# Optimization experiments

Hardware: AMD Instinct MI355X
Metric: run time of the kernel (lower is better)

The kernel has to match this reference:

```python
import jax, jax.numpy as jnp
import numpy as np
from jax import lax

B, C, H_CH, G = 4, 16, 128, 64
STOCH_RATE = 0.5
TWO_PI = np.float32(2.0 * np.pi)
ALIVE_THRESH = np.float32(0.1)


def _sobel_percep_kernel(c):
    # depthwise perception: [identity, sobel_x, sobel_y, sobel_z] per channel
    s = np.array([1.0, 2.0, 1.0], np.float32)
    d = np.array([-1.0, 0.0, 1.0], np.float32)
    ident = np.zeros((3, 3, 3), np.float32); ident[1, 1, 1] = 1.0
    sx = np.einsum('i,j,k->ijk', s, s, d)
    sy = np.einsum('i,j,k->ijk', s, d, s)
    sz = np.einsum('i,j,k->ijk', d, s, s)
    base = np.stack([ident, sx, sy, sz], 0)          # [4,3,3,3]
    k = np.tile(base, (c, 1, 1, 1))                  # [4C,3,3,3], group-major
    return jnp.asarray(k.reshape(4 * c, 1, 3, 3, 3))


def setup_inputs() -> dict:
    key = jax.random.key(0)
    k1, k2, k3, k4, k5 = jax.random.split(key, 5)
    x = jax.random.normal(k1, (B, C, G, G, G), jnp.float32)
    percep_kernel = _sobel_percep_kernel(C)          # [4C,1,3,3,3] fixed sobel stencils
    W1 = jax.random.normal(k2, (H_CH, 4 * C), jnp.float32) * 0.1
    b1 = jax.random.normal(k3, (H_CH,), jnp.float32) * 0.1
    W2 = jax.random.normal(k4, (C, H_CH), jnp.float32) * 0.1
    stoch_mask = jax.random.uniform(k5, (B, 1, G, G, G), jnp.float32)
    return {"x": x, "percep_kernel": percep_kernel, "W1": W1, "b1": b1,
            "W2": W2, "stoch_mask": stoch_mask}


def reference(x, percep_kernel, W1, b1, W2, stoch_mask):
    # alive mask: max_pool3d(alpha, k=3, s=1, p=1) > 0.1
    alpha = x[:, 3:4]
    pooled = lax.reduce_window(alpha, -jnp.inf, lax.max,
                               (1, 1, 3, 3, 3), (1, 1, 1, 1, 1), 'SAME')
    alive = (pooled > ALIVE_THRESH).astype(x.dtype)  # [B,1,D,H,W]
    # perception: depthwise 3x3x3 conv, 4 filters per channel
    p = lax.conv_general_dilated(x, percep_kernel, (1, 1, 1), 'SAME',
                                 feature_group_count=C,
                                 dimension_numbers=('NCDHW', 'OIDHW', 'NCDHW'))
    # per-voxel MLP: conv1 (1x1x1, bias) -> relu -> conv2 (1x1x1, no bias)
    h = jax.nn.relu(jnp.einsum('oc,bcdhw->bodhw', W1, p)
                    + b1[None, :, None, None, None])
    dx = jnp.einsum('oc,bcdhw->bodhw', W2, h)
    # stochastic residual update
    smask = (stoch_mask <= STOCH_RATE).astype(x.dtype)
    xn = x + dx * smask
    # orientation_channels == 1: mask states, wrap angle channel mod 2*pi
    states = xn[:, :-1] * alive
    angle = jnp.mod(xn[:, -1:], TWO_PI)
    return jnp.concatenate([states, angle], axis=1)
```

## Files before the change

### kernel.cpp

```cpp
#include <hip/hip_runtime.h>
#include <math.h>

#define Bc 4
#define Cc 16
#define Hc 128
#define Gc 64

#define TZ 4
#define TY 4
#define TXX 16
#define HZ (TZ + 2)
#define HY (TY + 2)
#define HXX (TXX + 2)
#define HALO_PER_C (HZ * HY * HXX)
#define CH_PER_PASS 8

__global__ __launch_bounds__(256, 2) void nca_fused(
    const float* __restrict__ x,
    const float* __restrict__ W1,
    const float* __restrict__ b1,
    const float* __restrict__ W2,
    const float* __restrict__ stoch,
    float* __restrict__ out)
{
    __shared__ float w1s[Hc * 64];
    __shared__ float w2ts[Hc * Cc];
    __shared__ float b1s[Hc];
    __shared__ float xs[CH_PER_PASS * HALO_PER_C];

    const int tid = threadIdx.x;

    int bid = blockIdx.x;
    const int xt = bid % (Gc / TXX); bid /= (Gc / TXX);
    const int yt = bid % (Gc / TY); bid /= (Gc / TY);
    const int zt = bid % (Gc / TZ); bid /= (Gc / TZ);
    const int b  = bid;

    const int z0 = zt * TZ, y0 = yt * TY, x0 = xt * TXX;

    {
        const float4* W1v = (const float4*)W1;
        float4* w1sv = (float4*)w1s;
#pragma unroll
        for (int i = 0; i < (Hc * 64 / 4) / 256; ++i)
            w1sv[tid + i * 256] = W1v[tid + i * 256];
        if (tid < Hc) b1s[tid] = b1[tid];
#pragma unroll
        for (int i = 0; i < (Cc * Hc) / 256; ++i) {
            const int idx = tid + i * 256;
            const int k = idx >> 7;
            const int h = idx & (Hc - 1);
            w2ts[h * Cc + k] = W2[idx];
        }
    }

    const int tx = tid % TXX;
    const int ty = (tid / TXX) % TY;
    const int tz = tid / (TXX * TY);

    float p[64];
    float pooled = -1e30f;

#pragma unroll
    for (int pass = 0; pass < 2; ++pass) {
        __syncthreads();
        for (int idx = tid; idx < CH_PER_PASS * HALO_PER_C; idx += 256) {
            int hx = idx % HXX;
            int t  = idx / HXX;
            int hy = t % HY; t /= HY;
            int hz = t % HZ;
            int cc = t / HZ;
            const int c = pass * CH_PER_PASS + cc;
            int gz = z0 + hz - 1, gy = y0 + hy - 1, gx = x0 + hx - 1;
            float v = 0.0f;
            if ((unsigned)gz < (unsigned)Gc && (unsigned)gy < (unsigned)Gc &&
                (unsigned)gx < (unsigned)Gc) {
                v = x[(((b * Cc + c) * Gc + gz) * Gc + gy) * Gc + gx];
            }
            xs[idx] = v;
        }
        __syncthreads();

#pragma unroll
        for (int cc = 0; cc < CH_PER_PASS; ++cc) {
            const int g = pass * CH_PER_PASS + cc;
            const float* xc = &xs[cc * HALO_PER_C];
            float S[3][3], D[3][3];
            float center = 0.0f;
#pragma unroll
            for (int dz = 0; dz < 3; ++dz) {
#pragma unroll
                for (int dy = 0; dy < 3; ++dy) {
                    const int base = (tz + dz) * (HY * HXX) + (ty + dy) * HXX + tx;
                    const float a  = xc[base + 0];
                    const float m  = xc[base + 1];
                    const float c2 = xc[base + 2];
                    S[dz][dy] = a + 2.0f * m + c2;
                    D[dz][dy] = c2 - a;
                    if (dz == 1 && dy == 1) center = m;
                    if (g == 3) pooled = fmaxf(pooled, fmaxf(fmaxf(a, m), c2));
                }
            }
            const float sx = (D[0][0] + 2.0f * D[0][1] + D[0][2])
                     + 2.0f * (D[1][0] + 2.0f * D[1][1] + D[1][2])
                     +        (D[2][0] + 2.0f * D[2][1] + D[2][2]);
            const float sy = (S[0][2] - S[0][0])
                     + 2.0f * (S[1][2] - S[1][0])
                     +        (S[2][2] - S[2][0]);
            const float sz = (S[2][0] + 2.0f * S[2][1] + S[2][2])
                           - (S[0][0] + 2.0f * S[0][1] + S[0][2]);
            p[4 * g + 0] = center;
            p[4 * g + 1] = sx;
            p[4 * g + 2] = sy;
            p[4 * g + 3] = sz;
        }
    }

    const float alive = (pooled > 0.1f) ? 1.0f : 0.0f;

    float dxv[16];
#pragma unroll
    for (int k = 0; k < 16; ++k) dxv[k] = 0.0f;

#pragma unroll 1
    for (int o = 0; o < Hc; o += 8) {
        float acc[8];
#pragma unroll
        for (int i = 0; i < 8; ++i) acc[i] = b1s[o + i];
#pragma unroll
        for (int i = 0; i < 8; ++i) {
            const float4* w4 = (const float4*)&w1s[(o + i) * 64];
#pragma unroll
            for (int c4 = 0; c4 < 16; ++c4) {
                const float4 w = w4[c4];
                acc[i] = fmaf(w.x, p[4 * c4 + 0], acc[i]);
                acc[i] = fmaf(w.y, p[4 * c4 + 1], acc[i]);
                acc[i] = fmaf(w.z, p[4 * c4 + 2], acc[i]);
                acc[i] = fmaf(w.w, p[4 * c4 + 3], acc[i]);
            }
        }
#pragma unroll
        for (int i = 0; i < 8; ++i) {
            const float h = fmaxf(acc[i], 0.0f);
            const float4* w2 = (const float4*)&w2ts[(o + i) * Cc];
#pragma unroll
            for (int k4 = 0; k4 < 4; ++k4) {
                const float4 w = w2[k4];
                dxv[4 * k4 + 0] = fmaf(w.x, h, dxv[4 * k4 + 0]);
                dxv[4 * k4 + 1] = fmaf(w.y, h, dxv[4 * k4 + 1]);
                dxv[4 * k4 + 2] = fmaf(w.z, h, dxv[4 * k4 + 2]);
                dxv[4 * k4 + 3] = fmaf(w.w, h, dxv[4 * k4 + 3]);
            }
        }
    }

    const int gz = z0 + tz, gy = y0 + ty, gx = x0 + tx;
    const int vox = ((b * Gc + gz) * Gc + gy) * Gc + gx;
    const float sm = (stoch[vox] <= 0.5f) ? 1.0f : 0.0f;

    const float TWO_PI_F = 6.2831854820251464844f;

#pragma unroll
    for (int k = 0; k < 16; ++k) {
        const float xn = p[4 * k] + dxv[k] * sm;
        float res;
        if (k < 15) {
            res = xn * alive;
        } else {
            res = fmodf(xn, TWO_PI_F);
            if (res < 0.0f) res += TWO_PI_F;
        }
        out[(((b * Cc + k) * Gc + gz) * Gc + gy) * Gc + gx] = res;
    }
}

extern "C" void kernel_launch(void* const* d_in, const int* in_sizes, int n_in,
                              void* d_out, int out_size, void* d_ws, size_t ws_size,
                              hipStream_t stream) {
    const float* x     = (const float*)d_in[0];
    const float* W1    = (const float*)d_in[2];
    const float* b1    = (const float*)d_in[3];
    const float* W2    = (const float*)d_in[4];
    const float* stoch = (const float*)d_in[5];
    float* out = (float*)d_out;

    const int nblocks = Bc * (Gc / TZ) * (Gc / TY) * (Gc / TXX);
    nca_fused<<<nblocks, 256, 0, stream>>>(x, W1, b1, W2, stoch, out);
}
```

Measured before the change: 602.6 us.

## Compute two voxels per thread to reuse shared-memory weight loads in MLP

New measurement: 996.2 us. +65.3%, slower.

```diff
diff --git a/kernel.cpp b/kernel.cpp
--- a/kernel.cpp
+++ b/kernel.cpp
@@ -8,12 +8,14 @@
 
 #define TZ 4
 #define TY 4
-#define TXX 16
+#define TXH 16
+#define TXX 32
 #define HZ (TZ + 2)
 #define HY (TY + 2)
 #define HXX (TXX + 2)
 #define HALO_PER_C (HZ * HY * HXX)
-#define CH_PER_PASS 8
+#define CH_PER_PASS 4
+#define NPASS (Cc / CH_PER_PASS)
 
 __global__ __launch_bounds__(256, 2) void nca_fused(
     const float* __restrict__ x,
@@ -31,9 +33,9 @@
     const int tid = threadIdx.x;
 
     int bid = blockIdx.x;
-    const int xt = bid % (Gc / TXX); bid /= (Gc / TXX);
-    const int yt = bid % (Gc / TY); bid /= (Gc / TY);
-    const int zt = bid % (Gc / TZ); bid /= (Gc / TZ);
+    const int xt = bid & 1; bid >>= 1;
+    const int yt = bid & 15; bid >>= 4;
+    const int zt = bid & 15; bid >>= 4;
     const int b  = bid;
 
     const int z0 = zt * TZ, y0 = yt * TY, x0 = xt * TXX;
@@ -54,15 +56,15 @@
         }
     }
 
-    const int tx = tid % TXX;
-    const int ty = (tid / TXX) % TY;
-    const int tz = tid / (TXX * TY);
-
-    float p[64];
-    float pooled = -1e30f;
-
-#pragma unroll
-    for (int pass = 0; pass < 2; ++pass) {
+    const int tx = tid & 15;
+    const int ty = (tid >> 4) & 3;
+    const int tz = tid >> 6;
+
+    float p0[64], p1[64];
+    float pool0 = -1e30f, pool1 = -1e30f;
+
+#pragma unroll
+    for (int pass = 0; pass < NPASS; ++pass) {
         __syncthreads();
         for (int idx = tid; idx < CH_PER_PASS * HALO_PER_C; idx += 256) {
             int hx = idx % HXX;
@@ -85,92 +87,135 @@
         for (int cc = 0; cc < CH_PER_PASS; ++cc) {
             const int g = pass * CH_PER_PASS + cc;
             const float* xc = &xs[cc * HALO_PER_C];
-            float S[3][3], D[3][3];
-            float center = 0.0f;
+            float S0[3][3], D0[3][3], S1[3][3], D1[3][3];
+            float c0 = 0.0f, c1 = 0.0f;
 #pragma unroll
             for (int dz = 0; dz < 3; ++dz) {
 #pragma unroll
                 for (int dy = 0; dy < 3; ++dy) {
                     const int base = (tz + dz) * (HY * HXX) + (ty + dy) * HXX + tx;
-                    const float a  = xc[base + 0];
-                    const float m  = xc[base + 1];
-                    const float c2 = xc[base + 2];
-                    S[dz][dy] = a + 2.0f * m + c2;
-                    D[dz][dy] = c2 - a;
-                    if (dz == 1 && dy == 1) center = m;
-                    if (g == 3) pooled = fmaxf(pooled, fmaxf(fmaxf(a, m), c2));
+                    const float a0 = xc[base + 0];
+                    const float m0 = xc[base + 1];
+                    const float q0 = xc[base + 2];
+                    const float a1 = xc[base + 16];
+                    const float m1 = xc[base + 17];
+                    const float q1 = xc[base + 18];
+                    S0[dz][dy] = a0 + 2.0f * m0 + q0;
+                    D0[dz][dy] = q0 - a0;
+                    S1[dz][dy] = a1 + 2.0f * m1 + q1;
+                    D1[dz][dy] = q1 - a1;
+                    if (dz == 1 && dy == 1) { c0 = m0; c1 = m1; }
+                    if (g == 3) {
+                        pool0 = fmaxf(pool0, fmaxf(fmaxf(a0, m0), q0));
+                        pool1 = fmaxf(pool1, fmaxf(fmaxf(a1, m1), q1));
+                    }
                 }
             }
-            const float sx = (D[0][0] + 2.0f * D[0][1] + D[0][2])
-                     + 2.0f * (D[1][0] + 2.0f * D[1][1] + D[1][2])
-                     +        (D[2][0] + 2.0f * D[2][1] + D[2][2]);
-            const float sy = (S[0][2] - S[0][0])
-                     + 2.0f * (S[1][2] - S[1][0])
-                     +        (S[2][2] - S[2][0]);
-            const float sz = (S[2][0] + 2.0f * S[2][1] + S[2][2])
-                           - (S[0][0] + 2.0f * S[0][1] + S[0][2]);
-            p[4 * g + 0] = center;
-            p[4 * g + 1] = sx;
-            p[4 * g + 2] = sy;
-            p[4 * g + 3] = sz;
-        }
-    }
-
-    const float alive = (pooled > 0.1f) ? 1.0f : 0.0f;
-
-    float dxv[16];
-#pragma unroll
-    for (int k = 0; k < 16; ++k) dxv[k] = 0.0f;
+            const float sx0 = (D0[0][0] + 2.0f * D0[0][1] + D0[0][2])
+                      + 2.0f * (D0[1][0] + 2.0f * D0[1][1] + D0[1][2])
+                      +        (D0[2][0] + 2.0f * D0[2][1] + D0[2][2]);
+            const float sy0 = (S0[0][2] - S0[0][0])
+                      + 2.0f * (S0[1][2] - S0[1][0])
+                      +        (S0[2][2] - S0[2][0]);
+            const float sz0 = (S0[2][0] + 2.0f * S0[2][1] + S0[2][2])
+                            - (S0[0][0] + 2.0f * S0[0][1] + S0[0][2]);
+            const float sx1 = (D1[0][0] + 2.0f * D1[0][1] + D1[0][2])
+                      + 2.0f * (D1[1][0] + 2.0f * D1[1][1] + D1[1][2])
+                      +        (D1[2][0] + 2.0f * D1[2][1] + D1[2][2]);
+            const float sy1 = (S1[0][2] - S1[0][0])
+                      + 2.0f * (S1[1][2] - S1[1][0])
+                      +        (S1[2][2] - S1[2][0]);
+            const float sz1 = (S1[2][0] + 2.0f * S1[2][1] + S1[2][2])
+                            - (S1[0][0] + 2.0f * S1[0][1] + S1[0][2]);
+            p0[4 * g + 0] = c0; p0[4 * g + 1] = sx0;
+            p0[4 * g + 2] = sy0; p0[4 * g + 3] = sz0;
+            p1[4 * g + 0] = c1; p1[4 * g + 1] = sx1;
+            p1[4 * g + 2] = sy1; p1[4 * g + 3] = sz1;
+        }
+    }
+
+    const float alive0 = (pool0 > 0.1f) ? 1.0f : 0.0f;
+    const float alive1 = (pool1 > 0.1f) ? 1.0f : 0.0f;
+
+    float dx0[16], dx1[16];
+#pragma unroll
+    for (int k = 0; k < 16; ++k) { dx0[k] = 0.0f; dx1[k] = 0.0f; }
+
+    const float4* w1sv  = (const float4*)w1s;
+    const float4* w2tsv = (const float4*)w2ts;
+    const float4* b1sv  = (const float4*)b1s;
 
 #pragma unroll 1
     for (int o = 0; o < Hc; o += 8) {
-        float acc[8];
-#pragma unroll
-        for (int i = 0; i < 8; ++i) acc[i] = b1s[o + i];
+        float acc0[8], acc1[8];
+        {
+            const float4 ba = b1sv[(o >> 2) + 0];
+            const float4 bb = b1sv[(o >> 2) + 1];
+            acc0[0] = ba.x; acc0[1] = ba.y; acc0[2] = ba.z; acc0[3] = ba.w;
+            acc0[4] = bb.x; acc0[5] = bb.y; acc0[6] = bb.z; acc0[7] = bb.w;
+#pragma unroll
+            for (int i = 0; i < 8; ++i) acc1[i] = acc0[i];
+        }
+        const float4* wb = w1sv + o * 16;
+#pragma unroll
+        for (int c4 = 0; c4 < 16; ++c4) {
+#pragma unroll
+            for (int i = 0; i < 8; ++i) {
+                const float4 w = wb[i * 16 + c4];
+                acc0[i] = fmaf(w.x, p0[4 * c4 + 0], acc0[i]);
+                acc0[i] = fmaf(w.y, p0[4 * c4 + 1], acc0[i]);
+                acc0[i] = fmaf(w.z, p0[4 * c4 + 2], acc0[i]);
+                acc0[i] = fmaf(w.w, p0[4 * c4 + 3], acc0[i]);
+                acc1[i] = fmaf(w.x, p1[4 * c4 + 0], acc1[i]);
+                acc1[i] = fmaf(w.y, p1[4 * c4 + 1], acc1[i]);
+                acc1[i] = fmaf(w.z, p1[4 * c4 + 2], acc1[i]);
+                acc1[i] = fmaf(w.w, p1[4 * c4 + 3], acc1[i]);
+            }
+        }
+        const float4* w2b = w2tsv + o * 4;
 #pragma unroll
         for (int i = 0; i < 8; ++i) {
-            const float4* w4 = (const float4*)&w1s[(o + i) * 64];
-#pragma unroll
-            for (int c4 = 0; c4 < 16; ++c4) {
-                const float4 w = w4[c4];
-                acc[i] = fmaf(w.x, p[4 * c4 + 0], acc[i]);
-                acc[i] = fmaf(w.y, p[4 * c4 + 1], acc[i]);
-                acc[i] = fmaf(w.z, p[4 * c4 + 2], acc[i]);
-                acc[i] = fmaf(w.w, p[4 * c4 + 3], acc[i]);
-            }
-        }
-#pragma unroll
-        for (int i = 0; i < 8; ++i) {
-            const float h = fmaxf(acc[i], 0.0f);
-            const float4* w2 = (const float4*)&w2ts[(o + i) * Cc];
+            const float h0 = fmaxf(acc0[i], 0.0f);
+            const float h1 = fmaxf(acc1[i], 0.0f);
 #pragma unroll
             for (int k4 = 0; k4 < 4; ++k4) {
-                const float4 w = w2[k4];
-                dxv[4 * k4 + 0] = fmaf(w.x, h, dxv[4 * k4 + 0]);
-                dxv[4 * k4 + 1] = fmaf(w.y, h, dxv[4 * k4 + 1]);
-                dxv[4 * k4 + 2] = fmaf(w.z, h, dxv[4 * k4 + 2]);
-                dxv[4 * k4 + 3] = fmaf(w.w, h, dxv[4 * k4 + 3]);
-            }
-        }
-    }
-
-    const int gz = z0 + tz, gy = y0 + ty, gx = x0 + tx;
-    const int vox = ((b * Gc + gz) * Gc + gy) * Gc + gx;
-    const float sm = (stoch[vox] <= 0.5f) ? 1.0f : 0.0f;
+                const float4 w = w2b[i * 4 + k4];
+                dx0[4 * k4 + 0] = fmaf(w.x, h0, dx0[4 * k4 + 0]);
+                dx0[4 * k4 + 1] = fmaf(w.y, h0, dx0[4 * k4 + 1]);
+                dx0[4 * k4 + 2] = fmaf(w.z, h0, dx0[4 * k4 + 2]);
+                dx0[4 * k4 + 3] = fmaf(w.w, h0, dx0[4 * k4 + 3]);
+                dx1[4 * k4 + 0] = fmaf(w.x, h1, dx1[4 * k4 + 0]);
+                dx1[4 * k4 + 1] = fmaf(w.y, h1, dx1[4 * k4 + 1]);
+                dx1[4 * k4 + 2] = fmaf(w.z, h1, dx1[4 * k4 + 2]);
+                dx1[4 * k4 + 3] = fmaf(w.w, h1, dx1[4 * k4 + 3]);
+            }
+        }
+    }
+
+    const int gz = z0 + tz, gy = y0 + ty;
+    const int gx0 = x0 + tx, gx1 = x0 + tx + 16;
+    const int vox0 = ((b * Gc + gz) * Gc + gy) * Gc + gx0;
+    const int vox1 = vox0 + 16;
+    const float sm0 = (stoch[vox0] <= 0.5f) ? 1.0f : 0.0f;
+    const float sm1 = (stoch[vox1] <= 0.5f) ? 1.0f : 0.0f;
 
     const float TWO_PI_F = 6.2831854820251464844f;
 
+    const int obase = (((b * Cc) * Gc + gz) * Gc + gy) * Gc;
 #pragma unroll
     for (int k = 0; k < 16; ++k) {
-        const float xn = p[4 * k] + dxv[k] * sm;
-        float res;
+        const float xn0 = p0[4 * k] + dx0[k] * sm0;
+        const float xn1 = p1[4 * k] + dx1[k] * sm1;
+        float r0, r1;
         if (k < 15) {
-            res = xn * alive;
+            r0 = xn0 * alive0;
+            r1 = xn1 * alive1;
         } else {
-            res = fmodf(xn, TWO_PI_F);
-            if (res < 0.0f) res += TWO_PI_F;
-        }
-        out[(((b * Cc + k) * Gc + gz) * Gc + gy) * Gc + gx] = res;
+            r0 = fmodf(xn0, TWO_PI_F); if (r0 < 0.0f) r0 += TWO_PI_F;
+            r1 = fmodf(xn1, TWO_PI_F); if (r1 < 0.0f) r1 += TWO_PI_F;
+        }
+        out[obase + k * (Gc * Gc * Gc) + gx0] = r0;
+        out[obase + k * (Gc * Gc * Gc) + gx1] = r1;
     }
 }
 
```

## Move per-voxel MLP onto bf16 MFMA with three-way split for fp32 accuracy

Applied to the files above, without the earlier changes.

New measurement: 1.033 ms. +71.5%, slower.

```diff
diff --git a/kernel.cpp b/kernel.cpp
--- a/kernel.cpp
+++ b/kernel.cpp
@@ -7,15 +7,47 @@
 #define Gc 64
 
 #define TZ 4
-#define TY 4
-#define TXX 16
-#define HZ (TZ + 2)
-#define HY (TY + 2)
-#define HXX (TXX + 2)
-#define HALO_PER_C (HZ * HY * HXX)
-#define CH_PER_PASS 8
-
-__global__ __launch_bounds__(256, 2) void nca_fused(
+#define TY 8
+#define TX 8
+#define HALO 600
+
+typedef __attribute__((ext_vector_type(8)))  short        short8;
+typedef __attribute__((ext_vector_type(16))) float        f32x16;
+typedef __attribute__((ext_vector_type(4)))  unsigned int uint4v;
+typedef __attribute__((ext_vector_type(2)))  int          int2v;
+
+union FragU { uint4v u4; short8 s8; unsigned int u[4]; };
+
+static __device__ __forceinline__ unsigned int cvt_pk_bf16(float a, float b) {
+    unsigned int r;
+    asm("v_cvt_pk_bf16_f32 %0, %1, %2" : "=v"(r) : "v"(a), "v"(b));
+    return r;
+}
+static __device__ __forceinline__ void swap32(unsigned int &a, unsigned int &b) {
+    int2v r = __builtin_amdgcn_permlane32_swap((int)a, (int)b, false, false);
+    a = (unsigned int)r.x;
+    b = (unsigned int)r.y;
+}
+static __device__ __forceinline__ float lo_bf(unsigned int w) {
+    union { unsigned int u; float f; } x; x.u = w << 16; return x.f;
+}
+static __device__ __forceinline__ float hi_bf(unsigned int w) {
+    union { unsigned int u; float f; } x; x.u = w & 0xffff0000u; return x.f;
+}
+static __device__ __forceinline__ void split3(float a, float b,
+                                              unsigned int &wh, unsigned int &wm,
+                                              unsigned int &wl) {
+    wh = cvt_pk_bf16(a, b);
+    float r0 = a - lo_bf(wh), r1 = b - hi_bf(wh);
+    wm = cvt_pk_bf16(r0, r1);
+    r0 -= lo_bf(wm); r1 -= hi_bf(wm);
+    wl = cvt_pk_bf16(r0, r1);
+}
+static __device__ __forceinline__ f32x16 MF(const FragU& A, const FragU& B, f32x16 C) {
+    return __builtin_amdgcn_mfma_f32_32x32x16_bf16(A.s8, B.s8, C, 0, 0, 0);
+}
+
+__global__ __launch_bounds__(256, 2) void nca_mfma(
     const float* __restrict__ x,
     const float* __restrict__ W1,
     const float* __restrict__ b1,
@@ -23,154 +55,243 @@
     const float* __restrict__ stoch,
     float* __restrict__ out)
 {
-    __shared__ float w1s[Hc * 64];
-    __shared__ float w2ts[Hc * Cc];
-    __shared__ float b1s[Hc];
-    __shared__ float xs[CH_PER_PASS * HALO_PER_C];
-
-    const int tid = threadIdx.x;
+    __shared__ uint4v w1f[48 * 64];
+    __shared__ uint4v w2f[24 * 32];
+    __shared__ float  b1s[Hc];
+    __shared__ float  xs[HALO];
+
+    const int tid  = threadIdx.x;
+    const int lane = tid & 63;
 
     int bid = blockIdx.x;
-    const int xt = bid % (Gc / TXX); bid /= (Gc / TXX);
-    const int yt = bid % (Gc / TY); bid /= (Gc / TY);
-    const int zt = bid % (Gc / TZ); bid /= (Gc / TZ);
+    const int xt = bid & 7;  bid >>= 3;
+    const int yt = bid & 7;  bid >>= 3;
+    const int zt = bid & 15; bid >>= 4;
     const int b  = bid;
-
-    const int z0 = zt * TZ, y0 = yt * TY, x0 = xt * TXX;
-
-    {
-        const float4* W1v = (const float4*)W1;
-        float4* w1sv = (float4*)w1s;
-#pragma unroll
-        for (int i = 0; i < (Hc * 64 / 4) / 256; ++i)
-            w1sv[tid + i * 256] = W1v[tid + i * 256];
-        if (tid < Hc) b1s[tid] = b1[tid];
-#pragma unroll
-        for (int i = 0; i < (Cc * Hc) / 256; ++i) {
-            const int idx = tid + i * 256;
-            const int k = idx >> 7;
-            const int h = idx & (Hc - 1);
-            w2ts[h * Cc + k] = W2[idx];
-        }
-    }
-
-    const int tx = tid % TXX;
-    const int ty = (tid / TXX) % TY;
-    const int tz = tid / (TXX * TY);
+    const int z0 = zt * TZ, y0 = yt * TY, x0 = xt * TX;
+
+#pragma unroll
+    for (int i = 0; i < 4; ++i) {
+        const int slot = tid + i * 256;
+        const int L  = slot & 63;
+        const int ks = (slot >> 6) & 3;
+        const int t  = slot >> 8;
+        const int row = 32 * t + (L & 31);
+        const int kb  = 16 * ks + 8 * (L >> 5);
+        const float* src = W1 + row * 64 + kb;
+        unsigned int h[4], m[4], l[4];
+#pragma unroll
+        for (int q = 0; q < 4; ++q) split3(src[2*q], src[2*q+1], h[q], m[q], l[q]);
+        w1f[((t*4+ks)*3+0)*64 + L] = (uint4v){h[0],h[1],h[2],h[3]};
+        w1f[((t*4+ks)*3+1)*64 + L] = (uint4v){m[0],m[1],m[2],m[3]};
+        w1f[((t*4+ks)*3+2)*64 + L] = (uint4v){l[0],l[1],l[2],l[3]};
+    }
+#pragma unroll
+    for (int i = 0; i < 3; ++i) {
+        const int e = tid + i * 256;
+        const int sub = e & 31, slot = e >> 5;
+        const int ks = slot / 3, lvl = slot % 3;
+        const int r = sub & 15, hh = sub >> 4;
+        const int kb = 16 * ks + 8 * hh;
+        const float* src = W2 + r * Hc + kb;
+        unsigned int w[4];
+#pragma unroll
+        for (int q = 0; q < 4; ++q) {
+            unsigned int h, m, l;
+            split3(src[2*q], src[2*q+1], h, m, l);
+            w[q] = (lvl == 0) ? h : ((lvl == 1) ? m : l);
+        }
+        w2f[slot*32 + sub] = (uint4v){w[0],w[1],w[2],w[3]};
+    }
+    if (tid < Hc) b1s[tid] = b1[tid];
+
+    const int tx = tid & 7;
+    const int ty = (tid >> 3) & 7;
+    const int tz = tid >> 6;
 
     float p[64];
     float pooled = -1e30f;
 
 #pragma unroll
-    for (int pass = 0; pass < 2; ++pass) {
+    for (int c = 0; c < 16; ++c) {
         __syncthreads();
-        for (int idx = tid; idx < CH_PER_PASS * HALO_PER_C; idx += 256) {
-            int hx = idx % HXX;
-            int t  = idx / HXX;
-            int hy = t % HY; t /= HY;
-            int hz = t % HZ;
-            int cc = t / HZ;
-            const int c = pass * CH_PER_PASS + cc;
-            int gz = z0 + hz - 1, gy = y0 + hy - 1, gx = x0 + hx - 1;
+        for (int idx = tid; idx < HALO; idx += 256) {
+            const int hz = idx / 100;
+            const int r2 = idx - hz * 100;
+            const int hy = r2 / 10;
+            const int hx = r2 - hy * 10;
+            const int gz = z0 + hz - 1, gy = y0 + hy - 1, gx = x0 + hx - 1;
             float v = 0.0f;
             if ((unsigned)gz < (unsigned)Gc && (unsigned)gy < (unsigned)Gc &&
-                (unsigned)gx < (unsigned)Gc) {
-                v = x[(((b * Cc + c) * Gc + gz) * Gc + gy) * Gc + gx];
-            }
+                (unsigned)gx < (unsigned)Gc)
+                v = x[(((b*Cc + c)*Gc + gz)*Gc + gy)*Gc + gx];
             xs[idx] = v;
         }
         __syncthreads();
-
-#pragma unroll
-        for (int cc = 0; cc < CH_PER_PASS; ++cc) {
-            const int g = pass * CH_PER_PASS + cc;
-            const float* xc = &xs[cc * HALO_PER_C];
-            float S[3][3], D[3][3];
-            float center = 0.0f;
-#pragma unroll
-            for (int dz = 0; dz < 3; ++dz) {
-#pragma unroll
-                for (int dy = 0; dy < 3; ++dy) {
-                    const int base = (tz + dz) * (HY * HXX) + (ty + dy) * HXX + tx;
-                    const float a  = xc[base + 0];
-                    const float m  = xc[base + 1];
-                    const float c2 = xc[base + 2];
-                    S[dz][dy] = a + 2.0f * m + c2;
-                    D[dz][dy] = c2 - a;
-                    if (dz == 1 && dy == 1) center = m;
-                    if (g == 3) pooled = fmaxf(pooled, fmaxf(fmaxf(a, m), c2));
-                }
-            }
-            const float sx = (D[0][0] + 2.0f * D[0][1] + D[0][2])
-                     + 2.0f * (D[1][0] + 2.0f * D[1][1] + D[1][2])
-                     +        (D[2][0] + 2.0f * D[2][1] + D[2][2]);
-            const float sy = (S[0][2] - S[0][0])
-                     + 2.0f * (S[1][2] - S[1][0])
-                     +        (S[2][2] - S[2][0]);
-            const float sz = (S[2][0] + 2.0f * S[2][1] + S[2][2])
-                           - (S[0][0] + 2.0f * S[0][1] + S[0][2]);
-            p[4 * g + 0] = center;
-            p[4 * g + 1] = sx;
-            p[4 * g + 2] = sy;
-            p[4 * g + 3] = sz;
-        }
-    }
-
-    const float alive = (pooled > 0.1f) ? 1.0f : 0.0f;
+        float S[3][3], D[3][3], center = 0.f;
+#pragma unroll
+        for (int dz = 0; dz < 3; ++dz)
+#pragma unroll
+            for (int dy = 0; dy < 3; ++dy) {
+                const int base = (tz+dz)*100 + (ty+dy)*10 + tx;
+                const float a = xs[base], m = xs[base+1], q = xs[base+2];
+                S[dz][dy] = a + 2.f*m + q;
+                D[dz][dy] = q - a;
+                if (dz == 1 && dy == 1) center = m;
+                if (c == 3) pooled = fmaxf(pooled, fmaxf(fmaxf(a, m), q));
+            }
+        const float sx = (D[0][0]+2.f*D[0][1]+D[0][2])
+                 + 2.f*(D[1][0]+2.f*D[1][1]+D[1][2])
+                 +      (D[2][0]+2.f*D[2][1]+D[2][2]);
+        const float sy = (S[0][2]-S[0][0]) + 2.f*(S[1][2]-S[1][0]) + (S[2][2]-S[2][0]);
+        const float sz = (S[2][0]+2.f*S[2][1]+S[2][2]) - (S[0][0]+2.f*S[0][1]+S[0][2]);
+        p[4*c+0] = center; p[4*c+1] = sx; p[4*c+2] = sy; p[4*c+3] = sz;
+    }
+
+    const float alive = (pooled > 0.1f) ? 1.f : 0.f;
+    const int gz = z0 + tz, gy = y0 + ty, gxx = x0 + tx;
+    const float sm = (stoch[((b*Gc+gz)*Gc+gy)*Gc+gxx] <= 0.5f) ? 1.f : 0.f;
+
+    const int hi5 = lane >> 5;
+
+    float dxA[8], dxB[8], dx0[8];
+
+#pragma unroll
+    for (int grp = 0; grp < 2; ++grp) {
+        f32x16 acc[4];
+#pragma unroll
+        for (int t = 0; t < 4; ++t)
+#pragma unroll
+            for (int r = 0; r < 16; ++r) acc[t][r] = 0.f;
+
+#pragma unroll
+        for (int ks = 0; ks < 4; ++ks) {
+            unsigned int bh[8], bm[8], bl[8];
+#pragma unroll
+            for (int j = 0; j < 8; ++j)
+                split3(p[16*ks+2*j], p[16*ks+2*j+1], bh[j], bm[j], bl[j]);
+            FragU Bh, Bm, Bl;
+#pragma unroll
+            for (int j = 0; j < 4; ++j) {
+                swap32(bh[j], bh[j+4]); Bh.u[j] = (grp == 0) ? bh[j] : bh[j+4];
+                swap32(bm[j], bm[j+4]); Bm.u[j] = (grp == 0) ? bm[j] : bm[j+4];
+                swap32(bl[j], bl[j+4]); Bl.u[j] = (grp == 0) ? bl[j] : bl[j+4];
+            }
+#pragma unroll
+            for (int t = 0; t < 4; ++t) {
+                FragU Ah, Am, Al;
+                Ah.u4 = w1f[((t*4+ks)*3+0)*64 + lane];
+                Am.u4 = w1f[((t*4+ks)*3+1)*64 + lane];
+                Al.u4 = w1f[((t*4+ks)*3+2)*64 + lane];
+                acc[t] = MF(Ah, Bm, acc[t]);
+                acc[t] = MF(Am, Bh, acc[t]);
+                acc[t] = MF(Ah, Bl, acc[t]);
+                acc[t] = MF(Am, Bm, acc[t]);
+                acc[t] = MF(Al, Bh, acc[t]);
+            }
+        }
+#pragma unroll
+        for (int ks = 0; ks < 4; ++ks) {
+            unsigned int bh[8];
+#pragma unroll
+            for (int j = 0; j < 8; ++j)
+                bh[j] = cvt_pk_bf16(p[16*ks+2*j], p[16*ks+2*j+1]);
+            FragU Bh;
+#pragma unroll
+            for (int j = 0; j < 4; ++j) {
+                swap32(bh[j], bh[j+4]); Bh.u[j] = (grp == 0) ? bh[j] : bh[j+4];
+            }
+#pragma unroll
+            for (int t = 0; t < 4; ++t) {
+                FragU Ah; Ah.u4 = w1f[((t*4+ks)*3+0)*64 + lane];
+                acc[t] = MF(Ah, Bh, acc[t]);
+            }
+        }
+#pragma unroll
+        for (int t = 0; t < 4; ++t)
+#pragma unroll
+            for (int r = 0; r < 16; ++r)
+                acc[t][r] = fmaxf(acc[t][r] + b1s[32*t + (r&3) + 8*(r>>2) + 4*hi5], 0.f);
+
+        f32x16 a2;
+#pragma unroll
+        for (int r = 0; r < 16; ++r) a2[r] = 0.f;
+
+#pragma unroll
+        for (int ks = 0; ks < 8; ++ks) {
+            const int t = ks >> 1, wb = (ks & 1) * 4;
+            unsigned int h_[4], m_[4], l_[4];
+#pragma unroll
+            for (int j = 0; j < 4; ++j)
+                split3(acc[t][2*(wb+j)], acc[t][2*(wb+j)+1], h_[j], m_[j], l_[j]);
+            swap32(h_[0], h_[2]); swap32(h_[1], h_[3]);
+            swap32(m_[0], m_[2]); swap32(m_[1], m_[3]);
+            swap32(l_[0], l_[2]); swap32(l_[1], l_[3]);
+            FragU Bh, Bm, Bl;
+#pragma unroll
+            for (int j = 0; j < 4; ++j) { Bh.u[j] = h_[j]; Bm.u[j] = m_[j]; Bl.u[j] = l_[j]; }
+            const int widx = hi5 * 16 + (lane & 15);
+            FragU Ah, Am, Al;
+            Ah.u4 = w2f[(ks*3+0)*32 + widx];
+            Am.u4 = w2f[(ks*3+1)*32 + widx];
+            Al.u4 = w2f[(ks*3+2)*32 + widx];
+            a2 = MF(Ah, Bm, a2);
+            a2 = MF(Am, Bh, a2);
+            a2 = MF(Ah, Bl, a2);
+            a2 = MF(Am, Bm, a2);
+            a2 = MF(Al, Bh, a2);
+        }
+#pragma unroll
+        for (int ks = 0; ks < 8; ++ks) {
+            const int t = ks >> 1, wb = (ks & 1) * 4;
+            unsigned int h_[4];
+#pragma unroll
+            for (int j = 0; j < 4; ++j)
+                h_[j] = cvt_pk_bf16(acc[t][2*(wb+j)], acc[t][2*(wb+j)+1]);
+            swap32(h_[0], h_[2]); swap32(h_[1], h_[3]);
+            FragU Bh;
+#pragma unroll
+            for (int j = 0; j < 4; ++j) Bh.u[j] = h_[j];
+            const int widx = hi5 * 16 + (lane & 15);
+            FragU Ah; Ah.u4 = w2f[(ks*3+0)*32 + widx];
+            a2 = MF(Ah, Bh, a2);
+        }
+
+        if (grp == 0) {
+#pragma unroll
+            for (int r = 0; r < 8; ++r) dx0[r] = a2[r];
+        } else {
+#pragma unroll
+            for (int r = 0; r < 8; ++r) {
+                unsigned int ta = __float_as_uint(dx0[r]);
+                unsigned int tb = __float_as_uint(a2[r]);
+                swap32(ta, tb);
+                dxA[r] = __uint_as_float(ta);
+                dxB[r] = __uint_as_float(tb);
+            }
+        }
+    }
 
     float dxv[16];
 #pragma unroll
-    for (int k = 0; k < 16; ++k) dxv[k] = 0.0f;
-
-#pragma unroll 1
-    for (int o = 0; o < Hc; o += 8) {
-        float acc[8];
-#pragma unroll
-        for (int i = 0; i < 8; ++i) acc[i] = b1s[o + i];
-#pragma unroll
-        for (int i = 0; i < 8; ++i) {
-            const float4* w4 = (const float4*)&w1s[(o + i) * 64];
-#pragma unroll
-            for (int c4 = 0; c4 < 16; ++c4) {
-                const float4 w = w4[c4];
-                acc[i] = fmaf(w.x, p[4 * c4 + 0], acc[i]);
-                acc[i] = fmaf(w.y, p[4 * c4 + 1], acc[i]);
-                acc[i] = fmaf(w.z, p[4 * c4 + 2], acc[i]);
-                acc[i] = fmaf(w.w, p[4 * c4 + 3], acc[i]);
-            }
-        }
-#pragma unroll
-        for (int i = 0; i < 8; ++i) {
-            const float h = fmaxf(acc[i], 0.0f);
-            const float4* w2 = (const float4*)&w2ts[(o + i) * Cc];
-#pragma unroll
-            for (int k4 = 0; k4 < 4; ++k4) {
-                const float4 w = w2[k4];
-                dxv[4 * k4 + 0] = fmaf(w.x, h, dxv[4 * k4 + 0]);
-                dxv[4 * k4 + 1] = fmaf(w.y, h, dxv[4 * k4 + 1]);
-                dxv[4 * k4 + 2] = fmaf(w.z, h, dxv[4 * k4 + 2]);
-                dxv[4 * k4 + 3] = fmaf(w.w, h, dxv[4 * k4 + 3]);
-            }
-        }
-    }
-
-    const int gz = z0 + tz, gy = y0 + ty, gx = x0 + tx;
-    const int vox = ((b * Gc + gz) * Gc + gy) * Gc + gx;
-    const float sm = (stoch[vox] <= 0.5f) ? 1.0f : 0.0f;
+    for (int r = 0; r < 8; ++r) {
+        const int c = (r&3) + 8*(r>>2);
+        dxv[c]   = dxA[r];
+        dxv[c+4] = dxB[r];
+    }
 
     const float TWO_PI_F = 6.2831854820251464844f;
-
-#pragma unroll
-    for (int k = 0; k < 16; ++k) {
-        const float xn = p[4 * k] + dxv[k] * sm;
+#pragma unroll
+    for (int c = 0; c < 16; ++c) {
+        const float xn = p[4*c] + dxv[c] * sm;
         float res;
-        if (k < 15) {
+        if (c < 15) {
             res = xn * alive;
         } else {
             res = fmodf(xn, TWO_PI_F);
-            if (res < 0.0f) res += TWO_PI_F;
-        }
-        out[(((b * Cc + k) * Gc + gz) * Gc + gy) * Gc + gx] = res;
+            if (res < 0.f) res += TWO_PI_F;
+        }
+        out[(((b*Cc + c)*Gc + gz)*Gc + gy)*Gc + gxx] = res;
     }
 }
 
@@ -184,6 +305,6 @@
     const float* stoch = (const float*)d_in[5];
     float* out = (float*)d_out;
 
-    const int nblocks = Bc * (Gc / TZ) * (Gc / TY) * (Gc / TXX);
-    nca_fused<<<nblocks, 256, 0, stream>>>(x, W1, b1, W2, stoch, out);
-}
+    const int nblocks = Bc * (Gc/TZ) * (Gc/TY) * (Gc/TX);
+    nca_mfma<<<nblocks, 256, 0, stream>>>(x, W1, b1, W2, stoch, out);
+}
```
